# Performance work log

Hardware: AMD Instinct MI355X
Metric: run time of the kernel (lower is better)

Reference implementation:

```python
import jax, jax.numpy as jnp
import numpy as np

N = 100000        # nodes
E = 1600000       # edges (no self loops)
NFEAT = 512
NHEADS = 3
NH1 = 8           # per-head out dim of layer 1 -> x1 has 24 cols
D1 = NHEADS * NH1
NCLASS = 32
LRELU = 0.2


def _seg_sum(vals, idx, n=N):
    return jax.ops.segment_sum(vals, idx, num_segments=n)


def _spmm(idx, vals, x):
    # sparse [N,N] @ dense [N,F]: out[i] = sum_{e: row=i} vals[e] * x[col[e]]
    return _seg_sum(vals[:, None] * x[idx[1]], idx[0])


def _relation(ft, nb, g1, g2, b1, b2, r):
    gamma = jax.nn.leaky_relu(ft @ g1 + nb @ g2, LRELU) + 1.0
    beta = jax.nn.leaky_relu(ft @ b1 + nb @ b2, LRELU)
    return ft + gamma * r + beta - nb          # transE-style m


def _gat_head(h, a, src, dst):
    # h: [N, out], a: [2*out]; edge-wise unnormalized attention then scatter-agg
    z = jnp.concatenate([h[src], h[dst]], axis=1) @ a          # [E']
    ee = jnp.exp(-jax.nn.leaky_relu(z, LRELU))                 # [E']
    rowsum = _seg_sum(ee, src)                                 # [N]
    hp = _seg_sum(ee[:, None] * h[dst], src) / rowsum[:, None] # [N, out]
    return jax.nn.elu(hp)                                      # concat=True path


def setup_inputs() -> dict:
    key = jax.random.key(0)
    ks = jax.random.split(key, 20)
    s = 0.05

    def w(k, shape):
        return jax.random.normal(k, shape, jnp.float32) * s

    x = jax.random.normal(ks[0], (N, NFEAT), jnp.float32)
    adj_indices = jax.random.randint(ks[1], (2, E), 0, N, dtype=jnp.int32)
    adj_values = jax.random.uniform(ks[2], (E,), jnp.float32)
    es = jax.random.randint(ks[3], (2, E + N), 0, N, dtype=jnp.int32)
    loops = jnp.arange(N, dtype=jnp.int32)
    adj_self_indices = es.at[:, E:].set(jnp.stack([loops, loops]))  # ensure self loops

    return {
        "x": x,
        "adj_values": adj_values,
        "w_g1": w(ks[4], (NFEAT, NFEAT)), "w_g2": w(ks[5], (NFEAT, NFEAT)),
        "w_b1": w(ks[6], (NFEAT, NFEAT)), "w_b2": w(ks[7], (NFEAT, NFEAT)),
        "r1_r": w(ks[8], (NFEAT,)),
        "gat1_W": w(ks[9], (NHEADS, NFEAT, NH1)),
        "gat1_a": w(ks[10], (NHEADS, 2 * NH1)),
        "w2_g1": w(ks[11], (D1, D1)), "w2_g2": w(ks[12], (D1, D1)),
        "w2_b1": w(ks[13], (D1, D1)), "w2_b2": w(ks[14], (D1, D1)),
        "r2_r": w(ks[15], (D1,)),
        "gat2_W": w(ks[16], (D1, NCLASS)),
        "gat2_a": w(ks[17], (2 * NCLASS,)),
        "adj_indices": adj_indices,
        "adj_self_indices": adj_self_indices,
        "head": 0,
    }


def reference(x, adj_values, w_g1, w_g2, w_b1, w_b2, r1_r, gat1_W, gat1_a,
              w2_g1, w2_g2, w2_b1, w2_b2, r2_r, gat2_W, gat2_a,
              adj_indices, adj_self_indices, head):
    src, dst = adj_self_indices[0], adj_self_indices[1]

    # ---- layer 1 (TailGAT_SP body), eval mode (dropout = identity) ----
    neighbor = _spmm(adj_indices, adj_values, x)
    m1 = _relation(x, neighbor, w_g1, w_g2, w_b1, w_b2, r1_r)
    hin = x if head else x + m1          # mi injected when not head (ablation=0)
    h = jnp.einsum('nf,hfo->hno', hin, gat1_W)                  # [3, N, 8]
    x1 = jax.vmap(lambda hh, aa: _gat_head(hh, aa, src, dst))(h, gat1_a)
    x1 = jnp.transpose(x1, (1, 0, 2)).reshape(N, D1)            # torch.cat(dim=1)
    x1 = jax.nn.elu(x1)

    # ---- layer 2 (TransGAT_SP, nheads=1) ----
    neighbor2 = _spmm(adj_indices, adj_values, x1)
    m2 = _relation(x1, neighbor2, w2_g1, w2_g2, w2_b1, w2_b2, r2_r)
    hin2 = x1 if head else x1 + m2
    x2 = _gat_head(hin2 @ gat2_W, gat2_a, src, dst)             # [N, nclass]

    return x2, jnp.linalg.norm(m1, axis=1), jnp.linalg.norm(m2, axis=1)
```

## Files before the change

kernel.cpp:

```cpp
#include <hip/hip_runtime.h>
#include <stdint.h>

typedef __bf16 bf16;
typedef __bf16 bf16x8 __attribute__((ext_vector_type(8)));
typedef float  f32x4  __attribute__((ext_vector_type(4)));

#define LRELU_S 0.2f

__device__ __forceinline__ float lrelu(float v){ return v > 0.f ? v : LRELU_S * v; }
__device__ __forceinline__ float eluf(float v){ return v > 0.f ? v : expm1f(v); }

__global__ void k_count(const int* __restrict__ adj, const int* __restrict__ selfe,
                        unsigned* __restrict__ cnt1, unsigned* __restrict__ cnt2, int E, int EN){
  int i = blockIdx.x * blockDim.x + threadIdx.x;
  if (i < E)  atomicAdd(&cnt1[adj[i]], 1u);
  if (i < EN) atomicAdd(&cnt2[selfe[i]], 1u);
}

__global__ void k_scan(unsigned* __restrict__ cnt, unsigned* __restrict__ rp, int n){
  __shared__ unsigned s[1024];
  int t = threadIdx.x;
  int chunk = (n + 1023) >> 10;
  int lo = t * chunk, hi = lo + chunk;
  if (lo > n) lo = n;
  if (hi > n) hi = n;
  unsigned sum = 0;
  for (int i = lo; i < hi; i++) sum += cnt[i];
  s[t] = sum; __syncthreads();
  for (int d = 1; d < 1024; d <<= 1){
    unsigned add = (t >= d) ? s[t - d] : 0u;
    __syncthreads();
    s[t] += add;
    __syncthreads();
  }
  unsigned run = s[t] - sum;
  for (int i = lo; i < hi; i++){ rp[i] = run; run += cnt[i]; cnt[i] = 0u; }
  if (hi == n) rp[n] = run;
}

__global__ void k_fill(const int* __restrict__ adj, const int* __restrict__ selfe,
                       const float* __restrict__ avals,
                       const unsigned* __restrict__ rp1, const unsigned* __restrict__ rp2,
                       unsigned* __restrict__ cur1, unsigned* __restrict__ cur2,
                       int* __restrict__ cols1, float* __restrict__ vals1,
                       int* __restrict__ dst2, int E, int EN){
  int i = blockIdx.x * blockDim.x + threadIdx.x;
  if (i < E){
    int r = adj[i];
    unsigned slot = rp1[r] + atomicAdd(&cur1[r], 1u);
    cols1[slot] = adj[E + i];
    vals1[slot] = avals[i];
  }
  if (i < EN){
    int sN = selfe[i];
    unsigned slot = rp2[sN] + atomicAdd(&cur2[sN], 1u);
    dst2[slot] = selfe[EN + i];
  }
}

__global__ void k_cvt_x(const float* __restrict__ x, bf16* __restrict__ xb, int n8){
  int i = blockIdx.x * blockDim.x + threadIdx.x;
  if (i >= n8) return;
  const f32x4* p = (const f32x4*)(x + (size_t)i * 8);
  f32x4 a = p[0], b = p[1];
  bf16x8 o;
  o[0]=(bf16)a[0]; o[1]=(bf16)a[1]; o[2]=(bf16)a[2]; o[3]=(bf16)a[3];
  o[4]=(bf16)b[0]; o[5]=(bf16)b[1]; o[6]=(bf16)b[2]; o[7]=(bf16)b[3];
  *(bf16x8*)(xb + (size_t)i * 8) = o;
}

__global__ void k_build_wt(const float* __restrict__ wg1, const float* __restrict__ wg2,
                           const float* __restrict__ wb1, const float* __restrict__ wb2,
                           bf16* __restrict__ Wt){
  int i = blockIdx.x * blockDim.x + threadIdx.x;
  int c = i >> 10, k = i & 1023;
  float v;
  if (c < 512) v = (k < 512) ? wg1[k * 512 + c] : wg2[(k - 512) * 512 + c];
  else { int cc = c - 512; v = (k < 512) ? wb1[k * 512 + cc] : wb2[(k - 512) * 512 + cc]; }
  Wt[(size_t)c * 1024 + k] = (bf16)v;
}

__global__ void k_build_w1b(const float* __restrict__ g1W, bf16* __restrict__ g1Wb){
  int i = blockIdx.x * blockDim.x + threadIdx.x;
  if (i >= 32 * 512) return;
  int c = i >> 9, k = i & 511;
  float v = 0.f;
  if (c < 24){ int h = c >> 3, o = c & 7; v = g1W[h * 4096 + k * 8 + o]; }
  g1Wb[i] = (bf16)v;
}

__global__ __launch_bounds__(256) void k_spmm1(const unsigned* __restrict__ rp, const int* __restrict__ cols,
    const float* __restrict__ vals, const bf16* __restrict__ xb, bf16* __restrict__ nbb, int N){
  int lane = threadIdx.x & 63;
  int r = blockIdx.x * 4 + (threadIdx.x >> 6);
  if (r >= N) return;
  unsigned b0 = rp[r], b1 = rp[r + 1];
  float acc[8] = {0.f,0.f,0.f,0.f,0.f,0.f,0.f,0.f};
  for (unsigned e = b0; e < b1; ++e){
    int c = cols[e]; float v = vals[e];
    bf16x8 xv = *(const bf16x8*)(xb + (size_t)c * 512 + lane * 8);
    #pragma unroll
    for (int j = 0; j < 8; j++) acc[j] += v * (float)xv[j];
  }
  bf16x8 o;
  #pragma unroll
  for (int j = 0; j < 8; j++) o[j] = (bf16)acc[j];
  *(bf16x8*)(nbb + (size_t)r * 512 + lane * 8) = o;
}

__global__ __launch_bounds__(256) void k_gemm1f(const bf16* __restrict__ xb, const bf16* __restrict__ nbb,
    const bf16* __restrict__ Wt, const float* __restrict__ r1, const int* __restrict__ headp,
    bf16* __restrict__ hinb, float* __restrict__ nrmsq, int M){
  __shared__ __align__(16) bf16 As[128 * 32];
  __shared__ __align__(16) bf16 Bg[128 * 32];
  __shared__ __align__(16) bf16 Bb[128 * 32];
  int bid = blockIdx.x;
  int chunk = gridDim.x >> 3;
  int tile = (bid & 7) * chunk + (bid >> 3);
  int rowBase = (tile >> 2) * 128;
  int fBase = (tile & 3) * 128;
  int tid = threadIdx.x, wave = tid >> 6, lane = tid & 63;
  int wm = wave >> 1, wn = wave & 1;
  f32x4 aG[4][4], aB[4][4];
  #pragma unroll
  for (int m = 0; m < 4; m++)
    #pragma unroll
    for (int n = 0; n < 4; n++){ aG[m][n] = (f32x4){0.f,0.f,0.f,0.f}; aB[m][n] = (f32x4){0.f,0.f,0.f,0.f}; }

  int sRow = wave * 16 + (lane >> 2);
  int sCol = (lane & 3) * 8;

  for (int kt = 0; kt < 32; ++kt){
    const bf16* Abase = (kt < 16) ? xb : nbb;
    int kcol = (kt & 15) * 32;
    #pragma unroll
    for (int c = 0; c < 2; c++){
      int rr = c * 64 + sRow;
      int grow = rowBase + rr; if (grow >= M) grow = M - 1;
      const bf16* asrc = Abase + (size_t)grow * 512 + kcol + sCol;
      __builtin_amdgcn_global_load_lds((const __attribute__((address_space(1))) void*)asrc,
          (__attribute__((address_space(3))) void*)&As[(size_t)(c * 64 + wave * 16) * 32], 16, 0, 0);
      const bf16* gsrc = Wt + (size_t)(fBase + rr) * 1024 + kt * 32 + sCol;
      __builtin_amdgcn_global_load_lds((const __attribute__((address_space(1))) void*)gsrc,
          (__attribute__((address_space(3))) void*)&Bg[(size_t)(c * 64 + wave * 16) * 32], 16, 0, 0);
      const bf16* bsrc = Wt + (size_t)(512 + fBase + rr) * 1024 + kt * 32 + sCol;
      __builtin_amdgcn_global_load_lds((const __attribute__((address_space(1))) void*)bsrc,
          (__attribute__((address_space(3))) void*)&Bb[(size_t)(c * 64 + wave * 16) * 32], 16, 0, 0);
    }
    __syncthreads();
    bf16x8 af[4], bg[4], bb[4];
    #pragma unroll
    for (int m = 0; m < 4; m++)
      af[m] = *(const bf16x8*)&As[(wm * 64 + m * 16 + (lane & 15)) * 32 + (lane >> 4) * 8];
    #pragma unroll
    for (int n = 0; n < 4; n++){
      bg[n] = *(const bf16x8*)&Bg[(wn * 64 + n * 16 + (lane & 15)) * 32 + (lane >> 4) * 8];
      bb[n] = *(const bf16x8*)&Bb[(wn * 64 + n * 16 + (lane & 15)) * 32 + (lane >> 4) * 8];
    }
    #pragma unroll
    for (int m = 0; m < 4; m++)
      #pragma unroll
      for (int n = 0; n < 4; n++){
        aG[m][n] = __builtin_amdgcn_mfma_f32_16x16x32_bf16(af[m], bg[n], aG[m][n], 0, 0, 0);
        aB[m][n] = __builtin_amdgcn_mfma_f32_16x16x32_bf16(af[m], bb[n], aB[m][n], 0, 0, 0);
      }
    __syncthreads();
  }

  int head = *headp;
  float rf[4];
  #pragma unroll
  for (int n = 0; n < 4; n++) rf[n] = r1[fBase + wn * 64 + n * 16 + (lane & 15)];
  #pragma unroll
  for (int m = 0; m < 4; m++){
    #pragma unroll
    for (int j = 0; j < 4; j++){
      int row = rowBase + wm * 64 + m * 16 + (lane >> 4) * 4 + j;
      bool ok = row < M;
      int rowc = ok ? row : M - 1;
      float msq = 0.f;
      #pragma unroll
      for (int n = 0; n < 4; n++){
        int f = fBase + wn * 64 + n * 16 + (lane & 15);
        float g = lrelu(aG[m][n][j]);
        float b = lrelu(aB[m][n][j]);
        float xf = (float)xb[(size_t)rowc * 512 + f];
        float nf = (float)nbb[(size_t)rowc * 512 + f];
        float mv = xf + (g + 1.f) * rf[n] + b - nf;
        msq += mv * mv;
        float hin = head ? xf : (xf + mv);
        if (ok) hinb[(size_t)row * 512 + f] = (bf16)hin;
      }
      #pragma unroll
      for (int d = 1; d < 16; d <<= 1) msq += __shfl_xor(msq, d);
      if (ok && (lane & 15) == 0) atomicAdd(&nrmsq[row], msq);
    }
  }
}

__global__ __launch_bounds__(256) void k_proj1(const bf16* __restrict__ hinb, const bf16* __restrict__ g1Wb,
    float* __restrict__ h1, int N){
  __shared__ __align__(16) bf16 Bs[32 * 520];
  __shared__ __align__(16) bf16 As[256 * 32];
  int tid = threadIdx.x, wave = tid >> 6, lane = tid & 63;
  #pragma unroll
  for (int i = 0; i < 8; i++){
    int e8 = tid + i * 256;
    int c = e8 >> 6, k = (e8 & 63) * 8;
    bf16x8 v = *(const bf16x8*)(g1Wb + c * 512 + k);
    *(bf16x8*)&Bs[c * 520 + k] = v;
  }
  int rBase = blockIdx.x * 256;
  f32x4 acc[4][2];
  #pragma unroll
  for (int m = 0; m < 4; m++){ acc[m][0] = (f32x4){0,0,0,0}; acc[m][1] = (f32x4){0,0,0,0}; }
  __syncthreads();
  for (int kt = 0; kt < 16; ++kt){
    #pragma unroll
    for (int i = 0; i < 4; i++){
      int r = (tid >> 2) + i * 64;
      int grow = rBase + r; if (grow >= N) grow = N - 1;
      const bf16* src = hinb + (size_t)grow * 512 + kt * 32 + (tid & 3) * 8;
      __builtin_amdgcn_global_load_lds((const __attribute__((address_space(1))) void*)src,
          (__attribute__((address_space(3))) void*)&As[(size_t)(i * 64 + wave * 16) * 32], 16, 0, 0);
    }
    __syncthreads();
    bf16x8 bf0 = *(const bf16x8*)&Bs[(0 * 16 + (lane & 15)) * 520 + kt * 32 + (lane >> 4) * 8];
    bf16x8 bf1 = *(const bf16x8*)&Bs[(1 * 16 + (lane & 15)) * 520 + kt * 32 + (lane >> 4) * 8];
    #pragma unroll
    for (int m = 0; m < 4; m++){
      bf16x8 af = *(const bf16x8*)&As[(wave * 64 + m * 16 + (lane & 15)) * 32 + (lane >> 4) * 8];
      acc[m][0] = __builtin_amdgcn_mfma_f32_16x16x32_bf16(af, bf0, acc[m][0], 0, 0, 0);
      acc[m][1] = __builtin_amdgcn_mfma_f32_16x16x32_bf16(af, bf1, acc[m][1], 0, 0, 0);
    }
    __syncthreads();
  }
  #pragma unroll
  for (int m = 0; m < 4; m++)
    #pragma unroll
    for (int n = 0; n < 2; n++)
      #pragma unroll
      for (int j = 0; j < 4; j++){
        int row = rBase + wave * 64 + m * 16 + (lane >> 4) * 4 + j;
        int col = n * 16 + (lane & 15);
        if (row < N) h1[(size_t)row * 32 + col] = acc[m][n][j];
      }
}

__global__ __launch_bounds__(256) void k_att1(const float* __restrict__ h1, const float* __restrict__ g1a,
    const float* __restrict__ nrmsq, float* __restrict__ a1s, float* __restrict__ a1d,
    float* __restrict__ nrm1, int N){
  int lane = threadIdx.x & 63;
  int r = blockIdx.x * 4 + (threadIdx.x >> 6);
  if (r >= N) return;
  if (lane < 24){
    float hv = h1[(size_t)r * 32 + lane];
    int h = lane >> 3, o = lane & 7;
    float ps = hv * g1a[h * 16 + o];
    float pd = hv * g1a[h * 16 + 8 + o];
    #pragma unroll
    for (int d = 1; d < 8; d <<= 1){ ps += __shfl_xor(ps, d); pd += __shfl_xor(pd, d); }
    if (o == 0){ a1s[r * 4 + h] = ps; a1d[r * 4 + h] = pd; }
  } else if (lane == 24){
    nrm1[r] = sqrtf(nrmsq[r]);
  }
}

__global__ __launch_bounds__(256) void k_gat1(const unsigned* __restrict__ rp2, const int* __restrict__ dst2,
    const float* __restrict__ h1, const float* __restrict__ a1s, const float* __restrict__ a1d,
    float* __restrict__ x1, int N){
  int lane = threadIdx.x & 63;
  int r = blockIdx.x * 4 + (threadIdx.x >> 6);
  if (r >= N) return;
  int cl = (lane < 24) ? lane : 0;
  int h = cl >> 3;
  float as = a1s[r * 4 + h];
  unsigned b0 = rp2[r], b1 = rp2[r + 1];
  float hp = 0.f, rs = 0.f;
  for (unsigned e = b0; e < b1; ++e){
    int d = dst2[e];
    float z = as + a1d[d * 4 + h];
    float ee = expf(-lrelu(z));
    hp += ee * h1[(size_t)d * 32 + cl];
    rs += ee;
  }
  if (lane < 24){
    float v = hp / rs;
    v = eluf(v); v = eluf(v);
    x1[(size_t)r * 24 + lane] = v;
  }
}

__global__ __launch_bounds__(256) void k_spmm2(const unsigned* __restrict__ rp, const int* __restrict__ cols,
    const float* __restrict__ vals, const float* __restrict__ x1, float* __restrict__ nb2, int N){
  int lane = threadIdx.x & 63;
  int r = blockIdx.x * 4 + (threadIdx.x >> 6);
  if (r >= N) return;
  int cl = (lane < 24) ? lane : 0;
  unsigned b0 = rp[r], b1 = rp[r + 1];
  float acc = 0.f;
  for (unsigned e = b0; e < b1; ++e)
    acc += vals[e] * x1[(size_t)cols[e] * 24 + cl];
  if (lane < 24) nb2[(size_t)r * 24 + lane] = acc;
}

__global__ void k_rel2(const float* __restrict__ x1, const float* __restrict__ nb2,
    const float* __restrict__ wg1, const float* __restrict__ wg2,
    const float* __restrict__ wb1, const float* __restrict__ wb2,
    const float* __restrict__ r2, const float* __restrict__ W2, const float* __restrict__ a2,
    const int* __restrict__ headp,
    float* __restrict__ hg, float* __restrict__ a2s, float* __restrict__ a2d,
    float* __restrict__ nrm2, int N){
  int r = blockIdx.x * blockDim.x + threadIdx.x;
  if (r >= N) return;
  int head = *headp;
  float xr[24], nr[24], hin[24];
  #pragma unroll
  for (int i = 0; i < 24; i++){ xr[i] = x1[(size_t)r*24+i]; nr[i] = nb2[(size_t)r*24+i]; }
  float nrm = 0.f;
  #pragma unroll
  for (int j = 0; j < 24; j++){
    float gp = 0.f, bp = 0.f;
    #pragma unroll
    for (int i = 0; i < 24; i++){
      gp += xr[i] * wg1[i*24+j] + nr[i] * wg2[i*24+j];
      bp += xr[i] * wb1[i*24+j] + nr[i] * wb2[i*24+j];
    }
    float m = xr[j] + (lrelu(gp) + 1.f) * r2[j] + lrelu(bp) - nr[j];
    nrm += m * m;
    hin[j] = head ? xr[j] : (xr[j] + m);
  }
  nrm2[r] = sqrtf(nrm);
  float as = 0.f, ad = 0.f;
  #pragma unroll
  for (int c = 0; c < 32; c++){
    float v = 0.f;
    #pragma unroll
    for (int i = 0; i < 24; i++) v += hin[i] * W2[i*32+c];
    hg[(size_t)r*32 + c] = v;
    as += v * a2[c]; ad += v * a2[32 + c];
  }
  a2s[r] = as; a2d[r] = ad;
}

__global__ __launch_bounds__(256) void k_gat2(const unsigned* __restrict__ rp2, const int* __restrict__ dst2,
    const float* __restrict__ hg, const float* __restrict__ a2s, const float* __restrict__ a2d,
    float* __restrict__ out, int N){
  int lane = threadIdx.x & 63;
  int r = blockIdx.x * 4 + (threadIdx.x >> 6);
  if (r >= N) return;
  int cl = lane & 31;
  float as = a2s[r];
  unsigned b0 = rp2[r], b1 = rp2[r + 1];
  float hp = 0.f, rs = 0.f;
  for (unsigned e = b0; e < b1; ++e){
    int d = dst2[e];
    float z = as + a2d[d];
    float ee = expf(-lrelu(z));
    hp += ee * hg[(size_t)d * 32 + cl];
    rs += ee;
  }
  if (lane < 32) out[(size_t)r * 32 + lane] = eluf(hp / rs);
}

extern "C" void kernel_launch(void* const* d_in, const int* in_sizes, int n_in,
                              void* d_out, int out_size, void* d_ws, size_t ws_size,
                              hipStream_t stream){
  const float* x     = (const float*)d_in[0];
  const float* avals = (const float*)d_in[1];
  const float* wg1   = (const float*)d_in[2];
  const float* wg2   = (const float*)d_in[3];
  const float* wb1   = (const float*)d_in[4];
  const float* wb2   = (const float*)d_in[5];
  const float* r1    = (const float*)d_in[6];
  const float* g1W   = (const float*)d_in[7];
  const float* g1a   = (const float*)d_in[8];
  const float* w2g1  = (const float*)d_in[9];
  const float* w2g2  = (const float*)d_in[10];
  const float* w2b1  = (const float*)d_in[11];
  const float* w2b2  = (const float*)d_in[12];
  const float* r2    = (const float*)d_in[13];
  const float* W2    = (const float*)d_in[14];
  const float* a2    = (const float*)d_in[15];
  const int*   adj   = (const int*)d_in[16];
  const int*   selfe = (const int*)d_in[17];
  const int*   headp = (const int*)d_in[18];

  const int N  = in_sizes[0] / 512;
  const int E  = in_sizes[1];
  const int EN = in_sizes[17] / 2;

  char* w = (char*)d_ws; size_t off = 0;
  auto carve = [&](size_t bytes) -> char* {
    char* p = w + off; off = (off + bytes + 255) & ~(size_t)255; return p;
  };
  unsigned* rp1   = (unsigned*)carve(((size_t)N + 1) * 4);
  unsigned* rp2   = (unsigned*)carve(((size_t)N + 1) * 4);
  unsigned* cnt1  = (unsigned*)carve(((size_t)N + 1) * 4);
  unsigned* cnt2  = (unsigned*)carve(((size_t)N + 1) * 4);
  int*      cols1 = (int*)carve((size_t)E * 4);
  float*    vals1 = (float*)carve((size_t)E * 4);
  int*      dst2  = (int*)carve((size_t)EN * 4);
  bf16*     xb    = (bf16*)carve((size_t)N * 512 * 2);
  bf16*     nbb   = (bf16*)carve((size_t)N * 512 * 2);
  bf16*     Wt    = (bf16*)carve((size_t)1024 * 1024 * 2);
  bf16*     g1Wb  = (bf16*)carve((size_t)32 * 512 * 2);
  bf16*     hinb  = (bf16*)carve((size_t)N * 512 * 2);
  float*    nrmsq = (float*)carve((size_t)N * 4);
  float*    h1    = (float*)carve((size_t)N * 32 * 4);
  float*    a1s   = (float*)carve((size_t)N * 4 * 4);
  float*    a1d   = (float*)carve((size_t)N * 4 * 4);
  float*    x1    = (float*)carve((size_t)N * 24 * 4);
  float*    nb2   = (float*)carve((size_t)N * 24 * 4);
  float*    hg    = (float*)carve((size_t)N * 32 * 4);
  float*    a2s   = (float*)carve((size_t)N * 4);
  float*    a2d   = (float*)carve((size_t)N * 4);

  float* out  = (float*)d_out;
  float* nrm1 = out + (size_t)N * 32;
  float* nrm2 = nrm1 + N;

  hipMemsetAsync(cnt1, 0, ((size_t)N + 1) * 4, stream);
  hipMemsetAsync(cnt2, 0, ((size_t)N + 1) * 4, stream);
  hipMemsetAsync(nrmsq, 0, (size_t)N * 4, stream);

  const int tb = 256;
  k_count<<<(EN + tb - 1) / tb, tb, 0, stream>>>(adj, selfe, cnt1, cnt2, E, EN);
  k_scan<<<1, 1024, 0, stream>>>(cnt1, rp1, N);
  k_scan<<<1, 1024, 0, stream>>>(cnt2, rp2, N);
  k_fill<<<(EN + tb - 1) / tb, tb, 0, stream>>>(adj, selfe, avals, rp1, rp2, cnt1, cnt2,
                                                cols1, vals1, dst2, E, EN);
  int n8 = N * 512 / 8;
  k_cvt_x<<<(n8 + tb - 1) / tb, tb, 0, stream>>>(x, xb, n8);
  k_build_wt<<<(1024 * 1024) / tb, tb, 0, stream>>>(wg1, wg2, wb1, wb2, Wt);
  k_build_w1b<<<(32 * 512) / tb, tb, 0, stream>>>(g1W, g1Wb);

  int rb = (N + 3) / 4;
  k_spmm1<<<rb, 256, 0, stream>>>(rp1, cols1, vals1, xb, nbb, N);

  int rowTiles = (N + 127) / 128;
  k_gemm1f<<<rowTiles * 4, 256, 0, stream>>>(xb, nbb, Wt, r1, headp, hinb, nrmsq, N);

  int pb = (N + 255) / 256;
  k_proj1<<<pb, 256, 0, stream>>>(hinb, g1Wb, h1, N);
  k_att1<<<rb, 256, 0, stream>>>(h1, g1a, nrmsq, a1s, a1d, nrm1, N);
  k_gat1<<<rb, 256, 0, stream>>>(rp2, dst2, h1, a1s, a1d, x1, N);
  k_spmm2<<<rb, 256, 0, stream>>>(rp1, cols1, vals1, x1, nb2, N);
  k_rel2<<<(N + tb - 1) / tb, tb, 0, stream>>>(x1, nb2, w2g1, w2g2, w2b1, w2b2, r2, W2, a2,
                                               headp, hg, a2s, a2d, nrm2, N);
  k_gat2<<<rb, 256, 0, stream>>>(rp2, dst2, hg, a2s, a2d, out, N);
}
```

Before: 2.767 ms.

## Double-buffer LDS tiles in relation GEMM and unroll SpMM gather by four

The relation GEMM now keeps two LDS buffers and issues the global-to-LDS loads for the next K tile before the MFMAs on the current one, so load latency can overlap compute and one barrier per iteration is dropped. The SpMM row loop is unrolled by four so four independent gathered feature loads are in flight per lane at once. Doubling the LDS footprint (48KB per block) may reduce how many blocks fit on a CU. A single barrier per iteration with async LDS loads relies on the loads having completed by that barrier.

```diff
diff --git a/kernel.cpp b/kernel.cpp
--- a/kernel.cpp
+++ b/kernel.cpp
@@ -96,7 +96,19 @@
   if (r >= N) return;
   unsigned b0 = rp[r], b1 = rp[r + 1];
   float acc[8] = {0.f,0.f,0.f,0.f,0.f,0.f,0.f,0.f};
-  for (unsigned e = b0; e < b1; ++e){
+  unsigned e = b0;
+  for (; e + 4 <= b1; e += 4){
+    int c0 = cols[e], c1 = cols[e+1], c2 = cols[e+2], c3 = cols[e+3];
+    float v0 = vals[e], v1 = vals[e+1], v2 = vals[e+2], v3 = vals[e+3];
+    bf16x8 x0 = *(const bf16x8*)(xb + (size_t)c0 * 512 + lane * 8);
+    bf16x8 x1 = *(const bf16x8*)(xb + (size_t)c1 * 512 + lane * 8);
+    bf16x8 x2 = *(const bf16x8*)(xb + (size_t)c2 * 512 + lane * 8);
+    bf16x8 x3 = *(const bf16x8*)(xb + (size_t)c3 * 512 + lane * 8);
+    #pragma unroll
+    for (int j = 0; j < 8; j++)
+      acc[j] += v0 * (float)x0[j] + v1 * (float)x1[j] + v2 * (float)x2[j] + v3 * (float)x3[j];
+  }
+  for (; e < b1; ++e){
     int c = cols[e]; float v = vals[e];
     bf16x8 xv = *(const bf16x8*)(xb + (size_t)c * 512 + lane * 8);
     #pragma unroll
@@ -111,9 +123,9 @@
 __global__ __launch_bounds__(256) void k_gemm1f(const bf16* __restrict__ xb, const bf16* __restrict__ nbb,
     const bf16* __restrict__ Wt, const float* __restrict__ r1, const int* __restrict__ headp,
     bf16* __restrict__ hinb, float* __restrict__ nrmsq, int M){
-  __shared__ __align__(16) bf16 As[128 * 32];
-  __shared__ __align__(16) bf16 Bg[128 * 32];
-  __shared__ __align__(16) bf16 Bb[128 * 32];
+  __shared__ __align__(16) bf16 As[2][128 * 32];
+  __shared__ __align__(16) bf16 Bg[2][128 * 32];
+  __shared__ __align__(16) bf16 Bb[2][128 * 32];
   int bid = blockIdx.x;
   int chunk = gridDim.x >> 3;
   int tile = (bid & 7) * chunk + (bid >> 3);
@@ -130,7 +142,7 @@
   int sRow = wave * 16 + (lane >> 2);
   int sCol = (lane & 3) * 8;
 
-  for (int kt = 0; kt < 32; ++kt){
+  auto stage = [&](int buf, int kt){
     const bf16* Abase = (kt < 16) ? xb : nbb;
     int kcol = (kt & 15) * 32;
     #pragma unroll
@@ -139,23 +151,29 @@
       int grow = rowBase + rr; if (grow >= M) grow = M - 1;
       const bf16* asrc = Abase + (size_t)grow * 512 + kcol + sCol;
       __builtin_amdgcn_global_load_lds((const __attribute__((address_space(1))) void*)asrc,
-          (__attribute__((address_space(3))) void*)&As[(size_t)(c * 64 + wave * 16) * 32], 16, 0, 0);
+          (__attribute__((address_space(3))) void*)&As[buf][(size_t)(c * 64 + wave * 16) * 32], 16, 0, 0);
       const bf16* gsrc = Wt + (size_t)(fBase + rr) * 1024 + kt * 32 + sCol;
       __builtin_amdgcn_global_load_lds((const __attribute__((address_space(1))) void*)gsrc,
-          (__attribute__((address_space(3))) void*)&Bg[(size_t)(c * 64 + wave * 16) * 32], 16, 0, 0);
+          (__attribute__((address_space(3))) void*)&Bg[buf][(size_t)(c * 64 + wave * 16) * 32], 16, 0, 0);
       const bf16* bsrc = Wt + (size_t)(512 + fBase + rr) * 1024 + kt * 32 + sCol;
       __builtin_amdgcn_global_load_lds((const __attribute__((address_space(1))) void*)bsrc,
-          (__attribute__((address_space(3))) void*)&Bb[(size_t)(c * 64 + wave * 16) * 32], 16, 0, 0);
-    }
-    __syncthreads();
+          (__attribute__((address_space(3))) void*)&Bb[buf][(size_t)(c * 64 + wave * 16) * 32], 16, 0, 0);
+    }
+  };
+
+  stage(0, 0);
+  __syncthreads();
+  int cur = 0;
+  for (int kt = 0; kt < 32; ++kt){
+    if (kt + 1 < 32) stage(cur ^ 1, kt + 1);
     bf16x8 af[4], bg[4], bb[4];
     #pragma unroll
     for (int m = 0; m < 4; m++)
-      af[m] = *(const bf16x8*)&As[(wm * 64 + m * 16 + (lane & 15)) * 32 + (lane >> 4) * 8];
+      af[m] = *(const bf16x8*)&As[cur][(wm * 64 + m * 16 + (lane & 15)) * 32 + (lane >> 4) * 8];
     #pragma unroll
     for (int n = 0; n < 4; n++){
-      bg[n] = *(const bf16x8*)&Bg[(wn * 64 + n * 16 + (lane & 15)) * 32 + (lane >> 4) * 8];
-      bb[n] = *(const bf16x8*)&Bb[(wn * 64 + n * 16 + (lane & 15)) * 32 + (lane >> 4) * 8];
+      bg[n] = *(const bf16x8*)&Bg[cur][(wn * 64 + n * 16 + (lane & 15)) * 32 + (lane >> 4) * 8];
+      bb[n] = *(const bf16x8*)&Bb[cur][(wn * 64 + n * 16 + (lane & 15)) * 32 + (lane >> 4) * 8];
     }
     #pragma unroll
     for (int m = 0; m < 4; m++)
@@ -165,6 +183,7 @@
         aB[m][n] = __builtin_amdgcn_mfma_f32_16x16x32_bf16(af[m], bb[n], aB[m][n], 0, 0, 0);
       }
     __syncthreads();
+    cur ^= 1;
   }
 
   int head = *headp;
```

Result: faster. 2.544 ms (-8.1%).
